# Kernel optimization log

Hardware: AMD Instinct MI355X
Metric: run time of the kernel (lower is better)

## Reference

```python
import jax, jax.numpy as jnp
import numpy as np

MARGIN = 0.2
ENCODER_STRIDE = 320


def setup_inputs() -> dict:
    key = jax.random.key(0)
    k1, k2, k3, k4 = jax.random.split(key, 4)
    B, D, T, NC = 8, 512, 2048, 4096
    student_features = jax.random.normal(k1, (B, D, T), dtype=jnp.float32)
    codebook = jax.random.normal(k2, (NC, D), dtype=jnp.float32)
    teacher_codes = jax.random.randint(k3, (B, T), 0, NC, dtype=jnp.int64)
    lengths = jax.random.randint(k4, (B,), 0, T * ENCODER_STRIDE, dtype=jnp.int64)
    return {
        "student_features": student_features,
        "teacher_codes": teacher_codes,
        "codebook": codebook,
        "lengths": lengths,
    }


def reference(student_features, teacher_codes, codebook, lengths):
    B, D, T = student_features.shape
    # frame-level valid mask: (B, T)
    frame_lengths = lengths // ENCODER_STRIDE
    mask = (jnp.arange(T)[None, :] < frame_lengths[:, None]).astype(student_features.dtype)

    # (B*T, D) flattened student vectors
    z = jnp.transpose(student_features, (0, 2, 1)).reshape(-1, D)

    # Euclidean cdist via ||z||^2 + ||c||^2 - 2 z c^T (matmul form, like torch.cdist)
    sq = (
        jnp.sum(z * z, axis=-1, keepdims=True)
        + jnp.sum(codebook * codebook, axis=-1)[None, :]
        - 2.0 * jnp.einsum("nd,cd->nc", z, codebook)
    )
    dists = jnp.sqrt(jnp.maximum(sq, 1e-12))  # (B*T, num_codes)

    teacher_flat = teacher_codes.reshape(-1)
    rows = jnp.arange(teacher_flat.shape[0])
    pos_dist = dists[rows, teacher_flat]
    # exclude the target code, then min over codebook
    dists_for_neg = dists.at[rows, teacher_flat].set(jnp.inf)
    neg_dist = jnp.min(dists_for_neg, axis=1)

    triplet = jax.nn.relu(pos_dist.reshape(B, T) - neg_dist.reshape(B, T) + MARGIN)
    loss = jnp.sum(triplet * mask) / (jnp.sum(mask) + 1e-8)
    return loss
```

## Files before the change

### kernel.cpp

```cpp
#include <hip/hip_runtime.h>
#include <hip/hip_bf16.h>

typedef float f32x4 __attribute__((ext_vector_type(4)));
typedef int v8i __attribute__((ext_vector_type(8)));

#define NB 8
#define ND 512
#define NT 2048
#define NCODES 4096
#define NM (NB * NT)
#define MARGIN_F 0.2f
#define ENC_STRIDE 320


static __device__ inline void async_copy16(const void* g, void* l) {
    __builtin_amdgcn_global_load_lds(
        (const __attribute__((address_space(1))) unsigned int*)g,
        (__attribute__((address_space(3))) unsigned int*)l, 16, 0, 0);
}

__global__ void prep_fused(const float* __restrict__ sf, const float* __restrict__ cb,
                           unsigned char* __restrict__ Zq, float* __restrict__ npart,
                           unsigned char* __restrict__ Cq, float* __restrict__ cnorm,
                           float* __restrict__ accum, unsigned int* __restrict__ ticket) {
    __shared__ float tile[128][65];
    __shared__ float redc[4][16];
    const int tid = threadIdx.x;
    const int wave = tid >> 6, lane = tid & 63, l15 = lane & 15, kq = lane >> 4;

    if (blockIdx.x < 1024) {
        const int bx = blockIdx.x;
        const int t0 = (bx & 31) * 64;
        const int d0 = ((bx >> 5) & 3) * 128;
        const int b = bx >> 7;
        const float* src = sf + (size_t)b * ND * NT;
#pragma unroll
        for (int it = 0; it < 8; it++) {
            int idx = it * 256 + tid;
            int d = idx >> 4, t4 = (idx & 15) * 4;
            float4 v = *(const float4*)(src + (size_t)(d0 + d) * NT + t0 + t4);
            tile[d][t4] = v.x; tile[d][t4 + 1] = v.y; tile[d][t4 + 2] = v.z; tile[d][t4 + 3] = v.w;
        }
        __syncthreads();
        const int m0 = b * NT + t0;
        {
            const int trow = wave * 16 + l15;
            unsigned char q[32];
#pragma unroll
            for (int j = 0; j < 32; j += 2) {
                float a = tile[kq * 32 + j][trow];
                float c = tile[kq * 32 + j + 1][trow];
                int p = __builtin_amdgcn_cvt_pk_fp8_f32(a, c, 0, false);
                q[j] = (unsigned char)(p & 0xFF);
                q[j + 1] = (unsigned char)((p >> 8) & 0xFF);
            }
            const int M_ = m0 >> 7, rg = ((m0 >> 4) & 7) + wave, K_ = d0 >> 7;
            char* base = (char*)Zq + ((size_t)((M_ * 4 + K_) * 8 + rg)) * 2048;
            *(uint4*)(base + lane * 16) = *(uint4*)&q[0];
            *(uint4*)(base + 1024 + lane * 16) = *(uint4*)&q[16];
        }
        if (tid < 64) {
            float s = 0.0f;
#pragma unroll 16
            for (int d = 0; d < 128; d++) {
                float v = tile[d][tid];
                s += v * v;
            }
            npart[(size_t)(d0 >> 7) * NM + m0 + tid] = s;
        }
    } else {
        if (blockIdx.x == 1279 && tid == 0) { *accum = 0.0f; *ticket = 0u; }
        const int r0 = (blockIdx.x - 1024) * 16;
        const int row = r0 + l15;
        const int K_ = wave;
        const float* src = cb + (size_t)row * ND + K_ * 128 + kq * 32;
        unsigned char q[32];
        float s = 0.0f;
#pragma unroll
        for (int j4 = 0; j4 < 8; j4++) {
            float4 v = *(const float4*)(src + j4 * 4);
            s += v.x * v.x + v.y * v.y + v.z * v.z + v.w * v.w;
            int p0 = __builtin_amdgcn_cvt_pk_fp8_f32(v.x, v.y, 0, false);
            int p1 = __builtin_amdgcn_cvt_pk_fp8_f32(v.z, v.w, 0, false);
            q[j4 * 4 + 0] = (unsigned char)(p0 & 0xFF);
            q[j4 * 4 + 1] = (unsigned char)((p0 >> 8) & 0xFF);
            q[j4 * 4 + 2] = (unsigned char)(p1 & 0xFF);
            q[j4 * 4 + 3] = (unsigned char)((p1 >> 8) & 0xFF);
        }
        const int N_ = r0 >> 7, rg = (r0 >> 4) & 7;
        char* base = (char*)Cq + ((size_t)((N_ * 4 + K_) * 8 + rg)) * 2048;
        *(uint4*)(base + lane * 16) = *(uint4*)&q[0];
        *(uint4*)(base + 1024 + lane * 16) = *(uint4*)&q[16];
        s += __shfl_xor(s, 16);
        s += __shfl_xor(s, 32);
        if (lane < 16) redc[wave][l15] = s;
        __syncthreads();
        if (tid < 16) cnorm[r0 + tid] = redc[0][tid] + redc[1][tid] + redc[2][tid] + redc[3][tid];
    }
}

__global__ __launch_bounds__(256, 2) void triplet_main(
    const unsigned char* __restrict__ Zq, const unsigned char* __restrict__ Cq,
    const float* __restrict__ cnorm, const int* __restrict__ teacher,
    float* __restrict__ negq, float* __restrict__ posq) {
    __shared__ __align__(16) unsigned char As[16384];
    __shared__ __align__(16) unsigned char Bs[16384];

    const int M_ = blockIdx.x;
    const int nq = blockIdx.y;
    const int m0 = M_ * 128;
    const int tid = threadIdx.x;
    const int wave = tid >> 6, lane = tid & 63;
    const int wr = wave >> 1, wc = wave & 1;
    const int l15 = lane & 15, quad = lane >> 4;

    const float INF = __builtin_inff();
    float minv[4][4], posv[4][4];
    int tch[4][4];
#pragma unroll
    for (int mi = 0; mi < 4; mi++)
#pragma unroll
        for (int r = 0; r < 4; r++) {
            minv[mi][r] = INF;
            posv[mi][r] = INF;
            tch[mi][r] = teacher[m0 + wr * 64 + mi * 16 + quad * 4 + r];
        }

    const char* gA0 = (const char*)Zq + (size_t)M_ * 4 * 16384 + wave * 4096 + lane * 16;
    char* lA = (char*)As + wave * 4096;
    char* lB = (char*)Bs + wave * 4096;

    for (int nt = 0; nt < 4; nt++) {
        const int N_ = nq * 4 + nt;
        const int n0 = N_ * 128;
        const char* gA = gA0;
        const char* gB = (const char*)Cq + (size_t)N_ * 4 * 16384 + wave * 4096 + lane * 16;
        f32x4 acc[4][4] = {};

        for (int kt = 0; kt < 4; kt++) {
#pragma unroll
            for (int i = 0; i < 4; i++) {
                async_copy16(gA + i * 1024, lA + i * 1024);
                async_copy16(gB + i * 1024, lB + i * 1024);
            }
            gA += 16384; gB += 16384;
            __syncthreads();

            v8i av[4], bv[4];
#pragma unroll
            for (int mi = 0; mi < 4; mi++) {
                int rg = wr * 4 + mi;
                union { uint4 q[2]; v8i v; } u;
                u.q[0] = *(const uint4*)(As + rg * 2048 + lane * 16);
                u.q[1] = *(const uint4*)(As + rg * 2048 + 1024 + lane * 16);
                av[mi] = u.v;
            }
#pragma unroll
            for (int ni = 0; ni < 4; ni++) {
                int rg = wc * 4 + ni;
                union { uint4 q[2]; v8i v; } u;
                u.q[0] = *(const uint4*)(Bs + rg * 2048 + lane * 16);
                u.q[1] = *(const uint4*)(Bs + rg * 2048 + 1024 + lane * 16);
                bv[ni] = u.v;
            }
#pragma unroll
            for (int mi = 0; mi < 4; mi++)
#pragma unroll
                for (int ni = 0; ni < 4; ni++)
                    acc[mi][ni] = __builtin_amdgcn_mfma_scale_f32_16x16x128_f8f6f4(
                        av[mi], bv[ni], acc[mi][ni], 0, 0,
                        0, 0x7F7F7F7F, 0, 0x7F7F7F7F);
            __syncthreads();
        }

        float cn[4]; int col[4];
#pragma unroll
        for (int ni = 0; ni < 4; ni++) {
            col[ni] = n0 + wc * 64 + ni * 16 + l15;
            cn[ni] = cnorm[col[ni]];
        }
#pragma unroll
        for (int mi = 0; mi < 4; mi++)
#pragma unroll
            for (int r = 0; r < 4; r++) {
                int t = tch[mi][r];
#pragma unroll
                for (int ni = 0; ni < 4; ni++) {
                    float val = fmaf(-2.0f, acc[mi][ni][r], cn[ni]);
                    bool ist = (col[ni] == t);
                    minv[mi][r] = fminf(minv[mi][r], ist ? INF : val);
                    posv[mi][r] = fminf(posv[mi][r], ist ? val : INF);
                }
            }
    }

    const int slot = nq * 2 + wc;
#pragma unroll
    for (int mi = 0; mi < 4; mi++)
#pragma unroll
        for (int r = 0; r < 4; r++) {
            float mn = minv[mi][r], ps = posv[mi][r];
#pragma unroll
            for (int off = 1; off < 16; off <<= 1) {
                mn = fminf(mn, __shfl_xor(mn, off));
                ps = fminf(ps, __shfl_xor(ps, off));
            }
            if (l15 == 0) {
                int m = m0 + wr * 64 + mi * 16 + quad * 4 + r;
                negq[(size_t)slot * NM + m] = mn;
                posq[(size_t)slot * NM + m] = ps;
            }
        }
}

__global__ void reduce_final(const float* __restrict__ negq, const float* __restrict__ posq,
                             const float* __restrict__ npart, const int* __restrict__ lengths,
                             float* __restrict__ accum, unsigned int* __restrict__ ticket,
                             float* __restrict__ out) {
    const float INF = __builtin_inff();
    const int m = blockIdx.x * 256 + threadIdx.x;
    float mn = INF, ps = INF;
#pragma unroll
    for (int s = 0; s < 16; s++) {
        mn = fminf(mn, negq[(size_t)s * NM + m]);
        ps = fminf(ps, posq[(size_t)s * NM + m]);
    }
    float zn = npart[m] + npart[NM + m] + npart[2 * NM + m] + npart[3 * NM + m];
    float negd = sqrtf(fmaxf(zn + mn, 1e-12f));
    float posd = sqrtf(fmaxf(zn + ps, 1e-12f));
    float tri = fmaxf(posd - negd + MARGIN_F, 0.0f);
    int b = m >> 11;
    int tt = m & (NT - 1);
    int flen = lengths[b] / ENC_STRIDE;
    float val = (tt < flen) ? tri : 0.0f;

    __shared__ float red[4];
#pragma unroll
    for (int off = 1; off < 64; off <<= 1) val += __shfl_xor(val, off);
    int lane = threadIdx.x & 63, w = threadIdx.x >> 6;
    if (lane == 0) red[w] = val;
    __syncthreads();
    if (threadIdx.x == 0) {
        atomicAdd(accum, red[0] + red[1] + red[2] + red[3]);
        __threadfence();
        unsigned int old = atomicAdd(ticket, 1u);
        if (old == 63u) {
            float total = atomicAdd(accum, 0.0f);
            float cnt = 0.0f;
            for (int bb = 0; bb < NB; bb++) cnt += (float)(lengths[bb] / ENC_STRIDE);
            out[0] = total / (cnt + 1e-8f);
        }
    }
}

extern "C" void kernel_launch(void* const* d_in, const int* in_sizes, int n_in,
                              void* d_out, int out_size, void* d_ws, size_t ws_size,
                              hipStream_t stream) {
    const float* sf = (const float*)d_in[0];
    const int* teacher = (const int*)d_in[1];
    const float* cb = (const float*)d_in[2];
    const int* lengths = (const int*)d_in[3];

    char* ws = (char*)d_ws;
    unsigned char* Zq = (unsigned char*)(ws);
    unsigned char* Cq = (unsigned char*)(ws + 8388608);
    float* cnorm = (float*)(ws + 10485760);
    float* npart = (float*)(ws + 10502144);
    float* negq = (float*)(ws + 10764288);
    float* posq = (float*)(ws + 11812864);
    float* accum = (float*)(ws + 12861440);
    unsigned int* ticket = (unsigned int*)(ws + 12861444);

    prep_fused<<<1280, 256, 0, stream>>>(sf, cb, Zq, npart, Cq, cnorm, accum, ticket);
    triplet_main<<<dim3(128, 8), 256, 0, stream>>>(Zq, Cq, cnorm, teacher, negq, posq);
    reduce_final<<<64, 256, 0, stream>>>(negq, posq, npart, lengths, accum, ticket,
                                         (float*)d_out);
}
```

Before: 135.0 us.

## Skip masked frame tiles and double-buffer LDS in the triplet GEMM

Prep blocks and main-kernel row tiles whose frames lie beyond each batch's valid length now exit early. Those rows are masked out of the loss, so their quantization and distance GEMM work is unnecessary. The main kernel also fuses the N and K loops into one pipelined loop with double-buffered LDS, issuing the next tile's async loads before computing the current one. The early exits leave the negq/posq/npart entries for skipped rows unwritten, which relies on reduce_final ignoring masked rows rather than multiplying possibly garbage values by zero.

```diff
diff --git a/kernel.cpp b/kernel.cpp
--- a/kernel.cpp
+++ b/kernel.cpp
@@ -20,6 +20,7 @@
 }
 
 __global__ void prep_fused(const float* __restrict__ sf, const float* __restrict__ cb,
+                           const int* __restrict__ lengths,
                            unsigned char* __restrict__ Zq, float* __restrict__ npart,
                            unsigned char* __restrict__ Cq, float* __restrict__ cnorm,
                            float* __restrict__ accum, unsigned int* __restrict__ ticket) {
@@ -33,6 +34,7 @@
         const int t0 = (bx & 31) * 64;
         const int d0 = ((bx >> 5) & 3) * 128;
         const int b = bx >> 7;
+        if (t0 >= lengths[b] / ENC_STRIDE) return;
         const float* src = sf + (size_t)b * ND * NT;
 #pragma unroll
         for (int it = 0; it < 8; it++) {
@@ -102,13 +104,17 @@
 __global__ __launch_bounds__(256, 2) void triplet_main(
     const unsigned char* __restrict__ Zq, const unsigned char* __restrict__ Cq,
     const float* __restrict__ cnorm, const int* __restrict__ teacher,
+    const int* __restrict__ lengths,
     float* __restrict__ negq, float* __restrict__ posq) {
-    __shared__ __align__(16) unsigned char As[16384];
-    __shared__ __align__(16) unsigned char Bs[16384];
+    __shared__ __align__(16) unsigned char As[2][16384];
+    __shared__ __align__(16) unsigned char Bs[2][16384];
 
     const int M_ = blockIdx.x;
+    const int m0 = M_ * 128;
+    const int flen = lengths[m0 >> 11] / ENC_STRIDE;
+    if ((m0 & (NT - 1)) >= flen) return;
+
     const int nq = blockIdx.y;
-    const int m0 = M_ * 128;
     const int tid = threadIdx.x;
     const int wave = tid >> 6, lane = tid & 63;
     const int wr = wave >> 1, wc = wave & 1;
@@ -126,72 +132,93 @@
             tch[mi][r] = teacher[m0 + wr * 64 + mi * 16 + quad * 4 + r];
         }
 
-    const char* gA0 = (const char*)Zq + (size_t)M_ * 4 * 16384 + wave * 4096 + lane * 16;
-    char* lA = (char*)As + wave * 4096;
-    char* lB = (char*)Bs + wave * 4096;
-
-    for (int nt = 0; nt < 4; nt++) {
-        const int N_ = nq * 4 + nt;
-        const int n0 = N_ * 128;
-        const char* gA = gA0;
-        const char* gB = (const char*)Cq + (size_t)N_ * 4 * 16384 + wave * 4096 + lane * 16;
-        f32x4 acc[4][4] = {};
-
-        for (int kt = 0; kt < 4; kt++) {
+    const int ldsoff = wave * 4096;
+    const char* gA0 = (const char*)Zq + (size_t)M_ * 4 * 16384 + ldsoff + lane * 16;
+    const char* gB0 = (const char*)Cq + (size_t)nq * 16 * 16384 + ldsoff + lane * 16;
+
+#pragma unroll
+    for (int i = 0; i < 4; i++) {
+        async_copy16(gA0 + i * 1024, (char*)As[0] + ldsoff + i * 1024);
+        async_copy16(gB0 + i * 1024, (char*)Bs[0] + ldsoff + i * 1024);
+    }
+    __syncthreads();
+
+    f32x4 acc[4][4];
+    int cur = 0;
+#pragma unroll 2
+    for (int u = 0; u < 16; ++u) {
+        const int nt = u >> 2, kt = u & 3;
+        if (kt == 0) {
+#pragma unroll
+            for (int mi = 0; mi < 4; mi++)
+#pragma unroll
+                for (int ni = 0; ni < 4; ni++)
+                    acc[mi][ni] = (f32x4){0.f, 0.f, 0.f, 0.f};
+        }
+        if (u < 15) {
+            const int un = u + 1;
+            const char* gA = gA0 + (size_t)(un & 3) * 16384;
+            const char* gB = gB0 + (size_t)un * 16384;
+            char* dA = (char*)As[cur ^ 1] + ldsoff;
+            char* dB = (char*)Bs[cur ^ 1] + ldsoff;
 #pragma unroll
             for (int i = 0; i < 4; i++) {
-                async_copy16(gA + i * 1024, lA + i * 1024);
-                async_copy16(gB + i * 1024, lB + i * 1024);
-            }
-            gA += 16384; gB += 16384;
-            __syncthreads();
-
-            v8i av[4], bv[4];
-#pragma unroll
-            for (int mi = 0; mi < 4; mi++) {
-                int rg = wr * 4 + mi;
-                union { uint4 q[2]; v8i v; } u;
-                u.q[0] = *(const uint4*)(As + rg * 2048 + lane * 16);
-                u.q[1] = *(const uint4*)(As + rg * 2048 + 1024 + lane * 16);
-                av[mi] = u.v;
-            }
+                async_copy16(gA + i * 1024, dA + i * 1024);
+                async_copy16(gB + i * 1024, dB + i * 1024);
+            }
+        }
+
+        const unsigned char* sA = As[cur];
+        const unsigned char* sB = Bs[cur];
+        v8i av[4], bv[4];
+#pragma unroll
+        for (int mi = 0; mi < 4; mi++) {
+            int rg = wr * 4 + mi;
+            union { uint4 q[2]; v8i v; } uu;
+            uu.q[0] = *(const uint4*)(sA + rg * 2048 + lane * 16);
+            uu.q[1] = *(const uint4*)(sA + rg * 2048 + 1024 + lane * 16);
+            av[mi] = uu.v;
+        }
+#pragma unroll
+        for (int ni = 0; ni < 4; ni++) {
+            int rg = wc * 4 + ni;
+            union { uint4 q[2]; v8i v; } uu;
+            uu.q[0] = *(const uint4*)(sB + rg * 2048 + lane * 16);
+            uu.q[1] = *(const uint4*)(sB + rg * 2048 + 1024 + lane * 16);
+            bv[ni] = uu.v;
+        }
+#pragma unroll
+        for (int mi = 0; mi < 4; mi++)
+#pragma unroll
+            for (int ni = 0; ni < 4; ni++)
+                acc[mi][ni] = __builtin_amdgcn_mfma_scale_f32_16x16x128_f8f6f4(
+                    av[mi], bv[ni], acc[mi][ni], 0, 0,
+                    0, 0x7F7F7F7F, 0, 0x7F7F7F7F);
+
+        if (kt == 3) {
+            const int n0 = (nq * 4 + nt) * 128;
+            float cn[4]; int col[4];
 #pragma unroll
             for (int ni = 0; ni < 4; ni++) {
-                int rg = wc * 4 + ni;
-                union { uint4 q[2]; v8i v; } u;
-                u.q[0] = *(const uint4*)(Bs + rg * 2048 + lane * 16);
-                u.q[1] = *(const uint4*)(Bs + rg * 2048 + 1024 + lane * 16);
-                bv[ni] = u.v;
+                col[ni] = n0 + wc * 64 + ni * 16 + l15;
+                cn[ni] = cnorm[col[ni]];
             }
 #pragma unroll
             for (int mi = 0; mi < 4; mi++)
 #pragma unroll
-                for (int ni = 0; ni < 4; ni++)
-                    acc[mi][ni] = __builtin_amdgcn_mfma_scale_f32_16x16x128_f8f6f4(
-                        av[mi], bv[ni], acc[mi][ni], 0, 0,
-                        0, 0x7F7F7F7F, 0, 0x7F7F7F7F);
-            __syncthreads();
-        }
-
-        float cn[4]; int col[4];
-#pragma unroll
-        for (int ni = 0; ni < 4; ni++) {
-            col[ni] = n0 + wc * 64 + ni * 16 + l15;
-            cn[ni] = cnorm[col[ni]];
-        }
-#pragma unroll
-        for (int mi = 0; mi < 4; mi++)
-#pragma unroll
-            for (int r = 0; r < 4; r++) {
-                int t = tch[mi][r];
-#pragma unroll
-                for (int ni = 0; ni < 4; ni++) {
-                    float val = fmaf(-2.0f, acc[mi][ni][r], cn[ni]);
-                    bool ist = (col[ni] == t);
-                    minv[mi][r] = fminf(minv[mi][r], ist ? INF : val);
-                    posv[mi][r] = fminf(posv[mi][r], ist ? val : INF);
+                for (int r = 0; r < 4; r++) {
+                    int t = tch[mi][r];
+#pragma unroll
+                    for (int ni = 0; ni < 4; ni++) {
+                        float val = fmaf(-2.0f, acc[mi][ni][r], cn[ni]);
+                        bool ist = (col[ni] == t);
+                        minv[mi][r] = fminf(minv[mi][r], ist ? INF : val);
+                        posv[mi][r] = fminf(posv[mi][r], ist ? val : INF);
+                    }
                 }
-            }
+        }
+        __syncthreads();
+        cur ^= 1;
     }
 
     const int slot = nq * 2 + wc;
@@ -271,8 +298,8 @@
     float* accum = (float*)(ws + 12861440);
     unsigned int* ticket = (unsigned int*)(ws + 12861444);
 
-    prep_fused<<<1280, 256, 0, stream>>>(sf, cb, Zq, npart, Cq, cnorm, accum, ticket);
-    triplet_main<<<dim3(128, 8), 256, 0, stream>>>(Zq, Cq, cnorm, teacher, negq, posq);
+    prep_fused<<<1280, 256, 0, stream>>>(sf, cb, lengths, Zq, npart, Cq, cnorm, accum, ticket);
+    triplet_main<<<dim3(128, 8), 256, 0, stream>>>(Zq, Cq, cnorm, teacher, lengths, negq, posq);
     reduce_final<<<64, 256, 0, stream>>>(negq, posq, npart, lengths, accum, ticket,
                                          (float*)d_out);
 }
```

Result: no change. 135.2 us (+0.1%).
